# Kernel tuning notes

Measured on AMD Instinct MI355X. Metric: run time of the kernel, lower is better.

Reference implementation:

```python
import jax, jax.numpy as jnp
import numpy as np

DIM = 256
HEADS = 8
HD = DIM // HEADS          # 32
WS = 8                     # window size
TOPK = 4
SCALE = HD ** -0.5


def setup_inputs() -> dict:
    key = jax.random.key(0)
    k1, k2, k3 = jax.random.split(key, 3)
    B, H, W = 8, 64, 64
    x = jax.random.normal(k1, (B, DIM, H, W), dtype=jnp.float32)
    # 1x1 conv weights (BN folded -> weight + bias), fan-in scaled to keep logits sane
    w_qkv = jax.random.normal(k2, (3 * DIM, DIM), dtype=jnp.float32) / np.sqrt(DIM)
    b_qkv = jnp.zeros((3 * DIM,), dtype=jnp.float32)
    w_proj = jax.random.normal(k3, (DIM, DIM), dtype=jnp.float32) / np.sqrt(DIM)
    b_proj = jnp.zeros((DIM,), dtype=jnp.float32)
    return {"x": x, "w_qkv": w_qkv, "b_qkv": b_qkv, "w_proj": w_proj, "b_proj": b_proj}


def _window_partition(t, ws):
    # t: [BH, D, H, W] -> [BH, R, ws*ws, D]
    bh, d, h, w = t.shape
    gh, gw = h // ws, w // ws
    t = t.reshape(bh, d, gh, ws, gw, ws)
    t = t.transpose(0, 2, 4, 3, 5, 1)          # [BH, gh, gw, ws, ws, D]
    return t.reshape(bh, gh * gw, ws * ws, d)


def reference(x, w_qkv, b_qkv, w_proj, b_proj):
    B, C, H, W = x.shape
    gh, gw = H // WS, W // WS
    R, T = gh * gw, WS * WS
    BH = B * HEADS

    # qkv 1x1 conv
    qkv = jnp.einsum('bchw,oc->bohw', x, w_qkv) + b_qkv[None, :, None, None]
    q, k, v = jnp.split(qkv, 3, axis=1)                       # each [B, C, H, W]

    def to_bh(t):
        return t.reshape(BH, HD, H, W)

    q_w = _window_partition(to_bh(q), WS)                     # [BH, R, T, HD]
    k_w = _window_partition(to_bh(k), WS)
    v_w = _window_partition(to_bh(v), WS)

    # region-level routing: mean-pooled region tokens
    q_r = q_w.mean(axis=2)                                    # [BH, R, HD]
    k_r = k_w.mean(axis=2)
    attn_r = jnp.einsum('brd,bkd->brk', q_r, k_r) * SCALE     # [BH, R, R]
    topk = min(TOPK, R)
    _, topk_idx = jax.lax.top_k(attn_r, topk)                 # [BH, R, K]

    # gather top-k key/value windows per query region
    bidx = jnp.arange(BH)[:, None, None]
    k_sel = k_w[bidx, topk_idx]                               # [BH, R, K, T, HD]
    v_sel = v_w[bidx, topk_idx]
    k_sel = k_sel.reshape(BH, R, topk * T, HD)
    v_sel = v_sel.reshape(BH, R, topk * T, HD)

    # token-level attention inside routed regions
    attn = jnp.einsum('brtd,brsd->brts', q_w, k_sel) * SCALE  # [BH, R, T, K*T]
    attn = jax.nn.softmax(attn, axis=-1)
    out_w = jnp.einsum('brts,brsd->brtd', attn, v_sel)        # [BH, R, T, HD]

    # window reverse -> [BH, HD, H, W]
    out = out_w.reshape(BH, gh, gw, WS, WS, HD)
    out = out.transpose(0, 5, 1, 3, 2, 4).reshape(BH, HD, H, W)
    out = out.reshape(B, C, H, W)

    out = jnp.einsum('bchw,oc->bohw', out, w_proj) + b_proj[None, :, None, None]
    return out
```

## Files before the change

kernel.cpp:

```cpp
#include <hip/hip_runtime.h>
#include <hip/hip_bf16.h>

#define ATT_SCALE 0.17677669529663687f
#define EXP_C1 0.2550349235534668f
#define EXP_C2 23.083120654223400f

typedef short v8s __attribute__((ext_vector_type(8)));
typedef float v4f __attribute__((ext_vector_type(4)));
typedef float v16f __attribute__((ext_vector_type(16)));
typedef const __attribute__((address_space(1))) unsigned int gu32;
typedef __attribute__((address_space(3))) unsigned int lu32;

__device__ __forceinline__ void g2l16(const void* g, void* l) {
  __builtin_amdgcn_global_load_lds((gu32*)g, (lu32*)l, 16, 0, 0);
}

__device__ __forceinline__ float bflo(unsigned u){ union{unsigned i;float f;}x; x.i=u<<16; return x.f; }
__device__ __forceinline__ float bfhi(unsigned u){ union{unsigned i;float f;}x; x.i=u&0xffff0000u; return x.f; }
__device__ __forceinline__ unsigned short bf16r(float v){
  __hip_bfloat16 h = __float2bfloat16(v);
  return *reinterpret_cast<unsigned short*>(&h);
}
__device__ __forceinline__ unsigned pack_bf2(float a, float b){
  return (unsigned)bf16r(a) | ((unsigned)bf16r(b) << 16);
}
__device__ __forceinline__ unsigned cvtpk(float lo, float hi){
  unsigned r;
  asm("v_cvt_pk_bf16_f32 %0, %1, %2" : "=v"(r) : "v"(lo), "v"(hi));
  return r;
}
__device__ __forceinline__ void pl32swap(unsigned &a, unsigned &b){
  asm volatile("v_permlane32_swap_b32 %0, %1" : "+v"(a), "+v"(b));
}

__global__ __launch_bounds__(256) void k_wprep(const float* __restrict__ w_qkv,
                                               const float* __restrict__ w_proj,
                                               unsigned short* __restrict__ Wq,
                                               unsigned short* __restrict__ Wp) {
  const int m = blockIdx.x, t = threadIdx.x;
  const float* src = (m < 768) ? (w_qkv + m*256) : (w_proj + (size_t)(m - 768)*256);
  unsigned short* dst = (m < 768) ? (Wq + m*256) : (Wp + (size_t)(m - 768)*256);
  int col = (t & ~63) | ((t & 63) ^ ((m & 7) << 3));
  dst[col] = bf16r(src[t]);
}

__global__ __launch_bounds__(256) void k_fqkv(
    const float* __restrict__ x,
    const unsigned short* __restrict__ Wq,
    const float* __restrict__ bias,
    unsigned short* __restrict__ qbuf, unsigned short* __restrict__ kbuf,
    unsigned short* __restrict__ vbuf, float* __restrict__ part) {
  __shared__ __align__(16) char lds[81920];
  const int tid = threadIdx.x;
  const int wv = tid >> 6, lane = tid & 63;
  const int nt = blockIdx.x;
  const int b = nt >> 6, pc = nt & 63;
  const int p0 = pc << 6;
  float* pbuf = (float*)(lds + 65536);

  const char* wlanebase = (const char*)Wq + ((size_t)(lane >> 3))*512 + (lane & 7)*16;

  auto stage = [&](int s2, int buf) {
    const int m2 = s2 >> 2, kt2 = s2 & 3;
    char* dst = lds + 32768 + buf*16384;
    #pragma unroll
    for (int o = 0; o < 4; ++o) {
      int op = wv*4 + o;
      g2l16(wlanebase + (size_t)(m2*128 + op*8)*512 + kt2*128, dst + op*1024);
    }
  };

  stage(0, 0);
  stage(1, 1);

  #pragma unroll
  for (int cc = 0; cc < 4; ++cc) {
    float hi[16];
    const float* xp = x + ((size_t)(b*256 + cc*64 + wv*16))*4096 + p0 + lane;
    #pragma unroll
    for (int i = 0; i < 16; ++i) hi[i] = xp[(size_t)i*4096];

    #pragma unroll
    for (int i = 0; i < 16; ++i) {
      float s = hi[i];
      s += __shfl_xor(s, 1);
      s += __shfl_xor(s, 2);
      s += __shfl_xor(s, 4);
      if ((lane & 7) == 0) pbuf[cc*512 + (wv*16 + i)*8 + (lane >> 3)] = s;
    }
    #pragma unroll
    for (int gi = 0; gi < 2; ++gi) {
      uint4 uh;
      uh.x = pack_bf2(hi[gi*8+0], hi[gi*8+1]); uh.y = pack_bf2(hi[gi*8+2], hi[gi*8+3]);
      uh.z = pack_bf2(hi[gi*8+4], hi[gi*8+5]); uh.w = pack_bf2(hi[gi*8+6], hi[gi*8+7]);
      int off = lane*512 + cc*128 + ((wv*32 + gi*16) ^ ((lane & 7) << 4));
      *(uint4*)(lds + off) = uh;
    }
  }
  __syncthreads();
  {
    const size_t pbase = (size_t)(b*64 + pc)*2048;
    #pragma unroll
    for (int s = 0; s < 8; ++s) part[pbase + s*256 + tid] = pbuf[s*256 + tid];
  }
  __syncthreads();

  auto epilogue = [&](int mm, v4f (*acc)[4]) {
    if (mm < 4) {
      unsigned short* outbuf = (mm < 2) ? qbuf : kbuf;
      #pragma unroll
      for (int i = 0; i < 2; ++i) {
        int o = mm*128 + wv*32 + i*16 + ((lane >> 4) << 2);
        int head = (o >> 5) & 7, d0 = o & 31;
        float b0 = bias[o], b1 = bias[o+1], b2 = bias[o+2], b3 = bias[o+3];
        #pragma unroll
        for (int j = 0; j < 4; ++j) {
          int p = nt*64 + j*16 + (lane & 15);
          int bb = p >> 12, ploc = p & 4095;
          int h = ploc >> 6, w = ploc & 63;
          int rr = ((h >> 3) << 3) | (w >> 3), tt = ((h & 7) << 3) | (w & 7);
          int bh = bb*8 + head;
          uint2 u;
          u.x = pack_bf2(acc[i][j][0] + b0, acc[i][j][1] + b1);
          u.y = pack_bf2(acc[i][j][2] + b2, acc[i][j][3] + b3);
          *(uint2*)(outbuf + (size_t)(((bh << 6) | rr)*64 + tt)*32 + d0) = u;
        }
      }
    } else {
      #pragma unroll
      for (int i = 0; i < 2; ++i) {
        int o = mm*128 + wv*32 + i*16 + ((lane >> 4) << 2);
        int vch = o - 512;
        int head = vch >> 5, d0 = vch & 31;
        float bv[4] = {bias[o], bias[o+1], bias[o+2], bias[o+3]};
        #pragma unroll
        for (int j = 0; j < 4; ++j) {
          int p = nt*64 + j*16 + (lane & 15);
          int bb = p >> 12, ploc = p & 4095;
          int h = ploc >> 6, w = ploc & 63;
          int rr = ((h >> 3) << 3) | (w >> 3), tt = ((h & 7) << 3) | (w & 7);
          int bh = bb*8 + head;
          size_t base = ((size_t)((bh << 6) | rr)*32 + d0)*64 + tt;
          #pragma unroll
          for (int c = 0; c < 4; ++c)
            vbuf[base + (size_t)c*64] = bf16r(acc[i][j][c] + bv[c]);
        }
      }
    }
  };

  v4f accA[2][4], accB[2][4];

  #pragma unroll
  for (int s = 0; s < 24; ++s) {
    const int m = s >> 2, kt = s & 3, cur = s % 3;
    v4f (*acc)[4] = (m & 1) ? accB : accA;
    if (kt == 0) {
      #pragma unroll
      for (int i = 0; i < 2; ++i)
        #pragma unroll
        for (int j = 0; j < 4; ++j) acc[i][j] = (v4f){0.f,0.f,0.f,0.f};
    }
    if (s < 22) stage(s + 2, (s + 2) % 3);
    if (kt == 0 && m > 0) {
      __builtin_amdgcn_sched_barrier(0);
      epilogue(m - 1, (m & 1) ? accA : accB);
      __builtin_amdgcn_sched_barrier(0);
    }
    {
      const char* wb = lds + 32768 + cur*16384;
      __builtin_amdgcn_s_setprio(1);
      #pragma unroll
      for (int kk = 0; kk < 2; ++kk) {
        const int kb = kk*64 + ((lane>>4)<<4);
        v8s a[2], bfr[4];
        #pragma unroll
        for (int i = 0; i < 2; ++i) {
          int mr = wv*32 + i*16 + (lane & 15);
          a[i] = *(const v8s*)(wb + mr*128 + (kb ^ ((mr & 7) << 4)));
        }
        #pragma unroll
        for (int j = 0; j < 4; ++j) {
          int nr = j*16 + (lane & 15);
          bfr[j] = *(const v8s*)(lds + nr*512 + kt*128 + (kb ^ ((nr & 7) << 4)));
        }
        #pragma unroll
        for (int i = 0; i < 2; ++i)
          #pragma unroll
          for (int j = 0; j < 4; ++j)
            acc[i][j] = __builtin_amdgcn_mfma_f32_16x16x32_bf16(a[i], bfr[j], acc[i][j], 0, 0, 0);
      }
      __builtin_amdgcn_s_setprio(0);
    }
    if (s < 23) {
      if (s == 20 || s == 21)                       asm volatile("s_waitcnt vmcnt(36)" ::: "memory");
      else if (s == 22)                             asm volatile("s_waitcnt vmcnt(0)"  ::: "memory");
      else if (s==4||s==5||s==8||s==9||s==12||s==13||s==16||s==17)
                                                    asm volatile("s_waitcnt vmcnt(12)" ::: "memory");
      else                                          asm volatile("s_waitcnt vmcnt(4)"  ::: "memory");
      __builtin_amdgcn_s_barrier();
      __builtin_amdgcn_sched_barrier(0);
    }
  }
  epilogue(5, accB);
}

__global__ __launch_bounds__(256) void k_xmr(const float* __restrict__ part,
                                             float* __restrict__ xmean) {
  const int blk = blockIdx.x;
  const int item = blk & 7;
  const int b = blk >> 6, rh = (blk >> 3) & 7;
  const int t = threadIdx.x;
  const int flat = item*256 + t;
  float acc = 0.f;
  const float* pp = part + (size_t)(b*64 + rh*8)*2048 + flat;
  #pragma unroll
  for (int j = 0; j < 8; ++j) acc += pp[(size_t)j*2048];
  const int c = flat >> 3, wc = flat & 7;
  xmean[(size_t)((b*256 + c) << 6) + (rh << 3) + wc] = acc * 0.015625f;
}

__global__ __launch_bounds__(256) void k_route(const float* __restrict__ xmean,
                                               const float* __restrict__ w_qkv,
                                               const float* __restrict__ b_qkv,
                                               int* __restrict__ topk) {
  __shared__ float xm[128][64];
  __shared__ float qr[64][33];
  __shared__ float kr[64][33];
  const int bh = blockIdx.x, b = bh >> 3, head = bh & 7;
  const int tid = threadIdx.x;
  const int d = tid & 31, r0 = tid >> 5;
  float qacc[8], kacc[8];
  const float bq = b_qkv[head*32 + d], bk = b_qkv[256 + head*32 + d];
  #pragma unroll
  for (int i = 0; i < 8; ++i) { qacc[i] = bq; kacc[i] = bk; }

  for (int c0 = 0; c0 < 256; c0 += 128) {
    __syncthreads();
    #pragma unroll
    for (int i = 0; i < 32; ++i) {
      int idx = i*256 + tid;
      int row = idx >> 6, col = idx & 63;
      xm[row][col] = xmean[(size_t)(b*256 + c0 + row)*64 + col];
    }
    __syncthreads();
    const float* wqp = w_qkv + (head*32 + d)*256 + c0;
    const float* wkp = w_qkv + (256 + head*32 + d)*256 + c0;
    for (int c = 0; c < 128; ++c) {
      float wq = wqp[c], wk = wkp[c];
      #pragma unroll
      for (int i = 0; i < 8; ++i) {
        float xv = xm[c][r0 + 8*i];
        qacc[i] += wq * xv;
        kacc[i] += wk * xv;
      }
    }
  }
  #pragma unroll
  for (int i = 0; i < 8; ++i) { qr[r0+8*i][d] = qacc[i]; kr[r0+8*i][d] = kacc[i]; }
  __syncthreads();

  float* ar = &xm[0][0];
  for (int item = tid; item < 4096; item += 256) {
    int i = item >> 6, j = item & 63;
    float s = 0.f;
    #pragma unroll
    for (int dd = 0; dd < 32; ++dd) s += qr[i][dd]*kr[j][dd];
    ar[i*64 + j] = s;
  }
  __syncthreads();
  if (tid < 64) {
    for (int kk = 0; kk < 4; ++kk) {
      float best = -3e38f; int bj = 0;
      for (int j = 0; j < 64; ++j) {
        float v = ar[tid*64 + j];
        if (v > best) { best = v; bj = j; }
      }
      ar[tid*64 + bj] = -3e38f;
      topk[(bh*64 + tid)*4 + kk] = bj;
    }
  }
}

__global__ __launch_bounds__(256) void k_proj(
    const unsigned short* __restrict__ Wp,
    const unsigned short* __restrict__ Bmat,
    const float* __restrict__ bias,
    float* __restrict__ outp) {
  __shared__ __align__(16) char lds[81920];
  const int tid = threadIdx.x;
  const int wv = tid >> 6, lane = tid & 63;
  const int nt = blockIdx.x;

  v4f acc[4][4];
  #pragma unroll
  for (int i = 0; i < 4; ++i)
    #pragma unroll
    for (int j = 0; j < 4; ++j) acc[i][j] = (v4f){0.f,0.f,0.f,0.f};

  const char* wlanebase = (const char*)Wp + ((size_t)(lane>>3))*512 + (lane&7)*16;
  const size_t prowlane = (size_t)(nt*64 + (lane>>3))*512 + (lane&7)*16;

  {
    #pragma unroll
    for (int o = 0; o < 8; ++o) {
      int op = wv*8 + o;
      g2l16(wlanebase + (size_t)(op*8)*512, lds + op*1024);
    }
    #pragma unroll
    for (int o = 0; o < 2; ++o) {
      int op = wv*2 + o;
      g2l16((const char*)Bmat + prowlane + (size_t)(op*8)*512, lds + 65536 + op*1024);
    }
    asm volatile("s_waitcnt vmcnt(0)" ::: "memory");
    __syncthreads();
  }

  #pragma unroll
  for (int kt = 0; kt < 4; ++kt) {
    const int cur = kt & 1;
    if (kt < 3) {
      const int k0b = (kt + 1)*128;
      char* wb = lds + (cur^1)*32768;
      char* xb = lds + 65536 + (cur^1)*8192;
      #pragma unroll
      for (int o = 0; o < 8; ++o) {
        int op = wv*8 + o;
        g2l16(wlanebase + (size_t)(op*8)*512 + k0b, wb + op*1024);
      }
      #pragma unroll
      for (int o = 0; o < 2; ++o) {
        int op = wv*2 + o;
        g2l16((const char*)Bmat + prowlane + (size_t)(op*8)*512 + k0b, xb + op*1024);
      }
    }
    const char* wb = lds + cur*32768;
    const char* xb = lds + 65536 + cur*8192;
    __builtin_amdgcn_s_setprio(1);
    #pragma unroll
    for (int kk = 0; kk < 2; ++kk) {
      const int kb = kk*64 + ((lane>>4)<<4);
      v8s a[4], b[4];
      #pragma unroll
      for (int i = 0; i < 4; ++i) {
        int mr = wv*64 + i*16 + (lane & 15);
        a[i] = *(const v8s*)(wb + mr*128 + (kb ^ ((mr & 7) << 4)));
      }
      #pragma unroll
      for (int j = 0; j < 4; ++j) {
        int nr = j*16 + (lane & 15);
        b[j] = *(const v8s*)(xb + nr*128 + (kb ^ ((nr & 7) << 4)));
      }
      #pragma unroll
      for (int i = 0; i < 4; ++i)
        #pragma unroll
        for (int j = 0; j < 4; ++j)
          acc[i][j] = __builtin_amdgcn_mfma_f32_16x16x32_bf16(a[i], b[j], acc[i][j], 0, 0, 0);
    }
    __builtin_amdgcn_s_setprio(0);
    if (kt < 3) {
      asm volatile("s_waitcnt vmcnt(0)" ::: "memory");
      __syncthreads();
    }
  }

  #pragma unroll
  for (int i = 0; i < 4; ++i) {
    int o = wv*64 + i*16 + ((lane >> 4) << 2);
    float b0 = bias[o], b1 = bias[o+1], b2 = bias[o+2], b3 = bias[o+3];
    #pragma unroll
    for (int j = 0; j < 4; ++j) {
      int p = nt*64 + j*16 + (lane & 15);
      int bb = p >> 12, ploc = p & 4095;
      float* dst = outp + ((size_t)(bb*256 + o))*4096 + ploc;
      dst[0]     = acc[i][j][0] + b0;
      dst[4096]  = acc[i][j][1] + b1;
      dst[8192]  = acc[i][j][2] + b2;
      dst[12288] = acc[i][j][3] + b3;
    }
  }
}

__global__ __launch_bounds__(256) void k_attn(const unsigned short* __restrict__ qw,
                                              const unsigned short* __restrict__ kw,
                                              const unsigned short* __restrict__ vwt,
                                              const int* __restrict__ topk,
                                              unsigned short* __restrict__ owt) {
  const int lane = threadIdx.x & 63;
  const int W = blockIdx.x*4 + (threadIdx.x >> 6);
  const int bh = W >> 6, rr = W & 63;
  const int lo5 = lane & 31, hi = lane >> 5;
  const int b = bh >> 3, head = bh & 7;

  const unsigned short* qb = qw + (size_t)(bh*64 + rr)*2048;
  v8s qf[2][2];
  #pragma unroll
  for (int qt = 0; qt < 2; ++qt)
    #pragma unroll
    for (int ck = 0; ck < 2; ++ck)
      qf[qt][ck] = *(const v8s*)(qb + (qt*32 + lo5)*32 + ck*16 + hi*8);

  int idx4[4];
  #pragma unroll
  for (int w = 0; w < 4; ++w) idx4[w] = topk[(bh*64 + rr)*4 + w];

  v16f O[2];
  #pragma unroll
  for (int qt = 0; qt < 2; ++qt)
    #pragma unroll
    for (int r = 0; r < 16; ++r) O[qt][r] = 0.f;
  float lsum[2] = {0.f, 0.f};

  #pragma unroll
  for (int w = 0; w < 4; ++w) {
    const unsigned short* kb = kw  + (size_t)(bh*64 + idx4[w])*2048;
    const unsigned short* vb = vwt + (size_t)(bh*64 + idx4[w])*2048;
    v8s kf[2][2], vf[4];
    #pragma unroll
    for (int kt = 0; kt < 2; ++kt)
      #pragma unroll
      for (int ck = 0; ck < 2; ++ck)
        kf[kt][ck] = *(const v8s*)(kb + (kt*32 + lo5)*32 + ck*16 + hi*8);
    #pragma unroll
    for (int mk = 0; mk < 4; ++mk)
      vf[mk] = *(const v8s*)(vb + lo5*64 + mk*16 + hi*8);

    v16f S[2][2];
    __builtin_amdgcn_s_setprio(1);
    #pragma unroll
    for (int kt = 0; kt < 2; ++kt)
      #pragma unroll
      for (int qt = 0; qt < 2; ++qt) {
        v16f z;
        #pragma unroll
        for (int r = 0; r < 16; ++r) z[r] = 0.f;
        z = __builtin_amdgcn_mfma_f32_32x32x16_bf16(kf[kt][0], qf[qt][0], z, 0, 0, 0);
        S[kt][qt] = __builtin_amdgcn_mfma_f32_32x32x16_bf16(kf[kt][1], qf[qt][1], z, 0, 0, 0);
      }
    __builtin_amdgcn_s_setprio(0);

    #pragma unroll
    for (int kt = 0; kt < 2; ++kt) {
      #pragma unroll
      for (int qt = 0; qt < 2; ++qt) {
        float p[16];
        #pragma unroll
        for (int r = 0; r < 16; ++r)
          p[r] = __builtin_amdgcn_exp2f(__builtin_fmaf(S[kt][qt][r], EXP_C1, -EXP_C2));
        float s01 = (p[0]+p[1]) + (p[2]+p[3]);
        float s23 = (p[4]+p[5]) + (p[6]+p[7]);
        float s45 = (p[8]+p[9]) + (p[10]+p[11]);
        float s67 = (p[12]+p[13]) + (p[14]+p[15]);
        lsum[qt] += (s01 + s23) + (s45 + s67);

        unsigned wh[8], wl[8];
        #pragma unroll
        for (int i = 0; i < 8; ++i) {
          wh[i] = cvtpk(p[2*i], p[2*i+1]);
          float l0 = p[2*i]   - bflo(wh[i]);
          float l1 = p[2*i+1] - bfhi(wh[i]);
          wl[i] = cvtpk(l0, l1);
        }
        pl32swap(wh[0], wh[2]); pl32swap(wh[1], wh[3]);
        pl32swap(wh[4], wh[6]); pl32swap(wh[5], wh[7]);
        pl32swap(wl[0], wl[2]); pl32swap(wl[1], wl[3]);
        pl32swap(wl[4], wl[6]); pl32swap(wl[5], wl[7]);
        union { unsigned u[4]; v8s v; } fA, fB;
        fA.u[0] = wh[0]; fA.u[1] = wh[1]; fA.u[2] = wh[2]; fA.u[3] = wh[3];
        fB.u[0] = wl[0]; fB.u[1] = wl[1]; fB.u[2] = wl[2]; fB.u[3] = wl[3];
        __builtin_amdgcn_s_setprio(1);
        O[qt] = __builtin_amdgcn_mfma_f32_32x32x16_bf16(fA.v, vf[2*kt], O[qt], 0, 0, 0);
        O[qt] = __builtin_amdgcn_mfma_f32_32x32x16_bf16(fB.v, vf[2*kt], O[qt], 0, 0, 0);
        __builtin_amdgcn_s_setprio(0);
        fA.u[0] = wh[4]; fA.u[1] = wh[5]; fA.u[2] = wh[6]; fA.u[3] = wh[7];
        fB.u[0] = wl[4]; fB.u[1] = wl[5]; fB.u[2] = wl[6]; fB.u[3] = wl[7];
        __builtin_amdgcn_s_setprio(1);
        O[qt] = __builtin_amdgcn_mfma_f32_32x32x16_bf16(fA.v, vf[2*kt+1], O[qt], 0, 0, 0);
        O[qt] = __builtin_amdgcn_mfma_f32_32x32x16_bf16(fB.v, vf[2*kt+1], O[qt], 0, 0, 0);
        __builtin_amdgcn_s_setprio(0);
      }
    }
  }

  float linv[2];
  #pragma unroll
  for (int qt = 0; qt < 2; ++qt) {
    float t = lsum[qt] + __shfl_xor(lsum[qt], 32);
    linv[qt] = 1.0f / t;
  }

  #pragma unroll
  for (int qt = 0; qt < 2; ++qt) {
    #pragma unroll
    for (int r = 0; r < 16; ++r) {
      int q = (r & 3) + 8*(r >> 2) + 4*hi;
      float li = __shfl(linv[qt], q);
      float val = O[qt][r] * li;
      int tok = qt*32 + q;
      int h = ((rr >> 3) << 3) | (tok >> 3);
      int wcol = ((rr & 7) << 3) | (tok & 7);
      int pg = (b << 12) | (h << 6) | wcol;
      int col = ((head >> 1) << 6) | ((((head & 1) << 5) + lo5) ^ ((tok & 7) << 3));
      owt[(size_t)pg*256 + col] = bf16r(val);
    }
  }
}

extern "C" void kernel_launch(void* const* d_in, const int* in_sizes, int n_in,
                              void* d_out, int out_size, void* d_ws, size_t ws_size,
                              hipStream_t stream) {
  (void)in_sizes; (void)n_in; (void)out_size; (void)ws_size;
  const float* x      = (const float*)d_in[0];
  const float* w_qkv  = (const float*)d_in[1];
  const float* b_qkv  = (const float*)d_in[2];
  const float* w_proj = (const float*)d_in[3];
  const float* b_proj = (const float*)d_in[4];
  float* out = (float*)d_out;

  char* ws = (char*)d_ws;
  unsigned short* owt = (unsigned short*)ws;
  unsigned short* Wq  = (unsigned short*)(ws + 16777216);
  unsigned short* Wp  = (unsigned short*)(ws + 17170432);
  unsigned short* qw  = (unsigned short*)(ws + 17301504);
  unsigned short* kw  = (unsigned short*)(ws + 34078720);
  unsigned short* vwt = (unsigned short*)(ws + 50855936);
  float* part         = (float*)(ws + 67633152);
  float* xmean        = (float*)(ws + 71827456);
  int* topk           = (int*)(ws + 72351744);

  k_wprep<<<dim3(1024), 256, 0, stream>>>(w_qkv, w_proj, Wq, Wp);
  k_fqkv <<<dim3(512),  256, 0, stream>>>(x, Wq, b_qkv, qw, kw, vwt, part);
  k_xmr  <<<dim3(512),  256, 0, stream>>>(part, xmean);
  k_route<<<dim3(64),   256, 0, stream>>>(xmean, w_qkv, b_qkv, topk);
  k_attn <<<dim3(1024), 256, 0, stream>>>(qw, kw, vwt, topk, owt);
  k_proj <<<dim3(512),  256, 0, stream>>>(Wp, owt, b_proj, out);
}
```

Baseline: 116.6 us.

## Fuse windowed attention with output projection through LDS

Merges the attention and projection kernels into one. Each 512-thread block handles one window for all 8 heads, stages the bf16 attention output in LDS, and then runs the 256x256 projection GEMM directly from LDS. This removes the global write and read-back of the intermediate attention output and one kernel launch. In exchange, the projection weight is no longer double-buffered, the block size and LDS footprint grow, and the projection loop waits at a barrier after every tile load.

After: 120.5 us. 1.03x slower.

```diff
diff --git a/kernel.cpp b/kernel.cpp
--- a/kernel.cpp
+++ b/kernel.cpp
@@ -282,115 +282,18 @@
   }
 }
 
-__global__ __launch_bounds__(256) void k_proj(
-    const unsigned short* __restrict__ Wp,
-    const unsigned short* __restrict__ Bmat,
-    const float* __restrict__ bias,
+__global__ __launch_bounds__(512) void k_fattn(
+    const unsigned short* __restrict__ qw, const unsigned short* __restrict__ kw,
+    const unsigned short* __restrict__ vwt, const int* __restrict__ topk,
+    const unsigned short* __restrict__ Wp, const float* __restrict__ bias,
     float* __restrict__ outp) {
-  __shared__ __align__(16) char lds[81920];
+  __shared__ __align__(16) char lds[65536];
   const int tid = threadIdx.x;
   const int wv = tid >> 6, lane = tid & 63;
-  const int nt = blockIdx.x;
-
-  v4f acc[4][4];
-  #pragma unroll
-  for (int i = 0; i < 4; ++i)
-    #pragma unroll
-    for (int j = 0; j < 4; ++j) acc[i][j] = (v4f){0.f,0.f,0.f,0.f};
-
-  const char* wlanebase = (const char*)Wp + ((size_t)(lane>>3))*512 + (lane&7)*16;
-  const size_t prowlane = (size_t)(nt*64 + (lane>>3))*512 + (lane&7)*16;
-
-  {
-    #pragma unroll
-    for (int o = 0; o < 8; ++o) {
-      int op = wv*8 + o;
-      g2l16(wlanebase + (size_t)(op*8)*512, lds + op*1024);
-    }
-    #pragma unroll
-    for (int o = 0; o < 2; ++o) {
-      int op = wv*2 + o;
-      g2l16((const char*)Bmat + prowlane + (size_t)(op*8)*512, lds + 65536 + op*1024);
-    }
-    asm volatile("s_waitcnt vmcnt(0)" ::: "memory");
-    __syncthreads();
-  }
-
-  #pragma unroll
-  for (int kt = 0; kt < 4; ++kt) {
-    const int cur = kt & 1;
-    if (kt < 3) {
-      const int k0b = (kt + 1)*128;
-      char* wb = lds + (cur^1)*32768;
-      char* xb = lds + 65536 + (cur^1)*8192;
-      #pragma unroll
-      for (int o = 0; o < 8; ++o) {
-        int op = wv*8 + o;
-        g2l16(wlanebase + (size_t)(op*8)*512 + k0b, wb + op*1024);
-      }
-      #pragma unroll
-      for (int o = 0; o < 2; ++o) {
-        int op = wv*2 + o;
-        g2l16((const char*)Bmat + prowlane + (size_t)(op*8)*512 + k0b, xb + op*1024);
-      }
-    }
-    const char* wb = lds + cur*32768;
-    const char* xb = lds + 65536 + cur*8192;
-    __builtin_amdgcn_s_setprio(1);
-    #pragma unroll
-    for (int kk = 0; kk < 2; ++kk) {
-      const int kb = kk*64 + ((lane>>4)<<4);
-      v8s a[4], b[4];
-      #pragma unroll
-      for (int i = 0; i < 4; ++i) {
-        int mr = wv*64 + i*16 + (lane & 15);
-        a[i] = *(const v8s*)(wb + mr*128 + (kb ^ ((mr & 7) << 4)));
-      }
-      #pragma unroll
-      for (int j = 0; j < 4; ++j) {
-        int nr = j*16 + (lane & 15);
-        b[j] = *(const v8s*)(xb + nr*128 + (kb ^ ((nr & 7) << 4)));
-      }
-      #pragma unroll
-      for (int i = 0; i < 4; ++i)
-        #pragma unroll
-        for (int j = 0; j < 4; ++j)
-          acc[i][j] = __builtin_amdgcn_mfma_f32_16x16x32_bf16(a[i], b[j], acc[i][j], 0, 0, 0);
-    }
-    __builtin_amdgcn_s_setprio(0);
-    if (kt < 3) {
-      asm volatile("s_waitcnt vmcnt(0)" ::: "memory");
-      __syncthreads();
-    }
-  }
-
-  #pragma unroll
-  for (int i = 0; i < 4; ++i) {
-    int o = wv*64 + i*16 + ((lane >> 4) << 2);
-    float b0 = bias[o], b1 = bias[o+1], b2 = bias[o+2], b3 = bias[o+3];
-    #pragma unroll
-    for (int j = 0; j < 4; ++j) {
-      int p = nt*64 + j*16 + (lane & 15);
-      int bb = p >> 12, ploc = p & 4095;
-      float* dst = outp + ((size_t)(bb*256 + o))*4096 + ploc;
-      dst[0]     = acc[i][j][0] + b0;
-      dst[4096]  = acc[i][j][1] + b1;
-      dst[8192]  = acc[i][j][2] + b2;
-      dst[12288] = acc[i][j][3] + b3;
-    }
-  }
-}
-
-__global__ __launch_bounds__(256) void k_attn(const unsigned short* __restrict__ qw,
-                                              const unsigned short* __restrict__ kw,
-                                              const unsigned short* __restrict__ vwt,
-                                              const int* __restrict__ topk,
-                                              unsigned short* __restrict__ owt) {
-  const int lane = threadIdx.x & 63;
-  const int W = blockIdx.x*4 + (threadIdx.x >> 6);
-  const int bh = W >> 6, rr = W & 63;
+  const int blk = blockIdx.x;
+  const int b = blk >> 6, rr = blk & 63;
+  const int head = wv, bh = b*8 + head;
   const int lo5 = lane & 31, hi = lane >> 5;
-  const int b = bh >> 3, head = bh & 7;
 
   const unsigned short* qb = qw + (size_t)(bh*64 + rr)*2048;
   v8s qf[2][2];
@@ -497,11 +400,65 @@
       float li = __shfl(linv[qt], q);
       float val = O[qt][r] * li;
       int tok = qt*32 + q;
-      int h = ((rr >> 3) << 3) | (tok >> 3);
-      int wcol = ((rr & 7) << 3) | (tok & 7);
-      int pg = (b << 12) | (h << 6) | wcol;
       int col = ((head >> 1) << 6) | ((((head & 1) << 5) + lo5) ^ ((tok & 7) << 3));
-      owt[(size_t)pg*256 + col] = bf16r(val);
+      *(unsigned short*)(lds + tok*512 + col*2) = bf16r(val);
+    }
+  }
+
+  const char* wlanebase = (const char*)Wp + ((size_t)(lane >> 3))*512 + (lane & 7)*16;
+  char* wlds = lds + 32768;
+
+  v4f acc[2][4];
+  #pragma unroll
+  for (int i = 0; i < 2; ++i)
+    #pragma unroll
+    for (int j = 0; j < 4; ++j) acc[i][j] = (v4f){0.f,0.f,0.f,0.f};
+
+  for (int kt = 0; kt < 4; ++kt) {
+    __syncthreads();
+    #pragma unroll
+    for (int o = 0; o < 4; ++o) {
+      int op = wv*4 + o;
+      g2l16(wlanebase + (size_t)(op*8)*512 + kt*128, wlds + op*1024);
+    }
+    __syncthreads();
+    __builtin_amdgcn_s_setprio(1);
+    #pragma unroll
+    for (int kk = 0; kk < 2; ++kk) {
+      const int kb = kk*64 + ((lane>>4)<<4);
+      v8s a[2], bfr[4];
+      #pragma unroll
+      for (int i = 0; i < 2; ++i) {
+        int mr = wv*32 + i*16 + (lane & 15);
+        a[i] = *(const v8s*)(wlds + mr*128 + (kb ^ ((mr & 7) << 4)));
+      }
+      #pragma unroll
+      for (int j = 0; j < 4; ++j) {
+        int nr = j*16 + (lane & 15);
+        bfr[j] = *(const v8s*)(lds + nr*512 + kt*128 + (kb ^ ((nr & 7) << 4)));
+      }
+      #pragma unroll
+      for (int i = 0; i < 2; ++i)
+        #pragma unroll
+        for (int j = 0; j < 4; ++j)
+          acc[i][j] = __builtin_amdgcn_mfma_f32_16x16x32_bf16(a[i], bfr[j], acc[i][j], 0, 0, 0);
+    }
+    __builtin_amdgcn_s_setprio(0);
+  }
+
+  #pragma unroll
+  for (int i = 0; i < 2; ++i) {
+    int o = wv*32 + i*16 + ((lane >> 4) << 2);
+    float b0 = bias[o], b1 = bias[o+1], b2 = bias[o+2], b3 = bias[o+3];
+    #pragma unroll
+    for (int j = 0; j < 4; ++j) {
+      int tok = j*16 + (lane & 15);
+      int ploc = (((rr >> 3) << 3) + (tok >> 3))*64 + ((rr & 7) << 3) + (tok & 7);
+      float* dst = outp + ((size_t)(b*256 + o))*4096 + ploc;
+      dst[0]     = acc[i][j][0] + b0;
+      dst[4096]  = acc[i][j][1] + b1;
+      dst[8192]  = acc[i][j][2] + b2;
+      dst[12288] = acc[i][j][3] + b3;
     }
   }
 }
@@ -518,7 +475,6 @@
   float* out = (float*)d_out;
 
   char* ws = (char*)d_ws;
-  unsigned short* owt = (unsigned short*)ws;
   unsigned short* Wq  = (unsigned short*)(ws + 16777216);
   unsigned short* Wp  = (unsigned short*)(ws + 17170432);
   unsigned short* qw  = (unsigned short*)(ws + 17301504);
@@ -532,6 +488,5 @@
   k_fqkv <<<dim3(512),  256, 0, stream>>>(x, Wq, b_qkv, qw, kw, vwt, part);
   k_xmr  <<<dim3(512),  256, 0, stream>>>(part, xmean);
   k_route<<<dim3(64),   256, 0, stream>>>(xmean, w_qkv, b_qkv, topk);
-  k_attn <<<dim3(1024), 256, 0, stream>>>(qw, kw, vwt, topk, owt);
-  k_proj <<<dim3(512),  256, 0, stream>>>(Wp, owt, b_proj, out);
-}
+  k_fattn<<<dim3(512),  512, 0, stream>>>(qw, kw, vwt, topk, Wp, b_proj, out);
+}
```
